# Kernel optimization log

Hardware: AMD Instinct MI355X
Metric: run time of the kernel (lower is better)

The kernel has to match this reference:

```python
import jax, jax.numpy as jnp
import numpy as np


def setup_inputs() -> dict:
    key = jax.random.key(0)
    ks = jax.random.split(key, 6)
    B, H, W, C = 4, 64, 64, 256
    D = 256  # d_model
    s = 0.02
    return {
        "features": jax.random.normal(ks[0], (B, H, W, C), dtype=jnp.float32),
        "Wq": jax.random.normal(ks[1], (C, D), dtype=jnp.float32) * s,
        "bq": jnp.zeros((D,), dtype=jnp.float32),
        "Wk": jax.random.normal(ks[2], (C, D), dtype=jnp.float32) * s,
        "bk": jnp.zeros((D,), dtype=jnp.float32),
        "Wv": jax.random.normal(ks[3], (C, D), dtype=jnp.float32) * s,
        "bv": jnp.zeros((D,), dtype=jnp.float32),
        "Wo": jax.random.normal(ks[4], (D, C), dtype=jnp.float32) * s,
        "bo": jnp.zeros((C,), dtype=jnp.float32),
    }


def reference(features, Wq, bq, Wk, bk, Wv, bv, Wo, bo):
    # features: [B, H, W, C] (NHWC). 1x1 convs are per-pixel GEMMs, so flatten
    # spatial dims to N = H*W tokens and do single-head self-attention.
    B, H, W, C = features.shape
    D = Wq.shape[1]
    x = features.reshape(B, H * W, C)          # [B, N, C]
    q = x @ Wq + bq                            # [B, N, D]
    k = x @ Wk + bk                            # [B, N, D]
    v = x @ Wv + bv                            # [B, N, D]
    scale = np.float32(1.0 / np.sqrt(D))
    scores = jnp.einsum("bnd,bmd->bnm", q, k) * scale   # [B, N, N]
    attn = jax.nn.softmax(scores, axis=-1)               # [B, N, N]
    out = jnp.einsum("bnm,bmd->bnd", attn, v)            # [B, N, D]
    out = out @ Wo + bo                                  # [B, N, C]
    return out.reshape(B, H, W, C)
```

## Files before the change

### kernel.cpp

```cpp
#include <hip/hip_runtime.h>
#include <hip/hip_bf16.h>


typedef __attribute__((ext_vector_type(8))) short short8;
typedef __attribute__((ext_vector_type(4))) short short4v;
typedef __attribute__((ext_vector_type(4))) float floatx4;

#define NB 4
#define NT 4096
#define CD 256
#define MTOT (NB * NT)

__device__ __forceinline__ short bf16s(float f) {
    union { float f; unsigned u; } a; a.f = f;
    unsigned u = a.u;
    return (short)((u + 0x7fffu + ((u >> 16) & 1u)) >> 16);
}

__device__ __forceinline__ float bf2f(short s) {
    union { unsigned u; float f; } a;
    a.u = ((unsigned)(unsigned short)s) << 16;
    return a.f;
}

__device__ __forceinline__ short8 ld8(const short* p) {
    return *(const short8*)p;
}

__device__ __forceinline__ floatx4 mfma16(short8 a, short8 b, floatx4 c) {
    return __builtin_amdgcn_mfma_f32_16x16x32_bf16(a, b, c, 0, 0, 0);
}

__device__ __forceinline__ void dma16(const void* g, void* l) {
    __builtin_amdgcn_global_load_lds(
        (const __attribute__((address_space(1))) void*)g,
        (__attribute__((address_space(3))) void*)l, 16, 0, 0);
}

__global__ __launch_bounds__(256) void k_convx(const float* __restrict__ x,
                                               short* __restrict__ xb) {
    int i = (blockIdx.x * 256 + threadIdx.x) * 4;
    float4 v = *(const float4*)(x + i);
    short4v o;
    o.x = bf16s(v.x); o.y = bf16s(v.y); o.z = bf16s(v.z); o.w = bf16s(v.w);
    *(short4v*)(xb + i) = o;
}

__global__ __launch_bounds__(256) void k_convw(const float* __restrict__ w0,
                                               const float* __restrict__ w1,
                                               const float* __restrict__ w2,
                                               const float* __restrict__ w3,
                                               short* __restrict__ wt) {
    int z = blockIdx.y;
    const float* w = (z == 0) ? w0 : (z == 1) ? w1 : (z == 2) ? w2 : w3;
    int c = blockIdx.x;
    int n = threadIdx.x;
    wt[z * 65536 + n * 256 + c] = bf16s(w[c * 256 + n]);
}

__global__ __launch_bounds__(256) void k_proj3(const short* __restrict__ A,
                                               const short* __restrict__ Wt,
                                               const float* __restrict__ bq,
                                               const float* __restrict__ bk,
                                               const float* __restrict__ bv,
                                               short* __restrict__ Qb,
                                               short* __restrict__ Kb,
                                               short* __restrict__ Vt) {
    __shared__ __align__(16) short Ws[16384];
    int blk = blockIdx.x;
    int wk = (blk & 7) * 192 + (blk >> 3);
    int m = wk / 12, rest = wk - m * 12;
    int z = rest >> 2, y = rest & 3;
    const short* W = Wt + z * 65536;
    const float* bias = (z == 0) ? bq : (z == 1) ? bk : bv;
    float scale = (z == 0) ? 0.0625f : 1.0f;
    int m0 = m * 128;
    int n0 = y * 64;
    int tid = threadIdx.x;
    int w = tid >> 6, l = tid & 63, r = l & 15, q = l >> 4;

#pragma unroll
    for (int cg = 0; cg < 8; ++cg)
        dma16(W + (size_t)(n0 + w * 16 + r) * CD + (cg * 4 + q) * 8,
              &Ws[w * 4096 + cg * 512]);
    __syncthreads();

    const short* a0 = A + (size_t)(m0 + w * 32 + r) * CD;
    const short* a1 = a0 + 16 * CD;
    floatx4 acc[2][4];
#pragma unroll
    for (int rt = 0; rt < 2; ++rt)
#pragma unroll
        for (int j = 0; j < 4; ++j) acc[rt][j] = (floatx4){0.f, 0.f, 0.f, 0.f};
#pragma unroll
    for (int c = 0; c < 8; ++c) {
        short8 af0 = ld8(a0 + c * 32 + q * 8);
        short8 af1 = ld8(a1 + c * 32 + q * 8);
#pragma unroll
        for (int j = 0; j < 4; ++j) {
            short8 wf = ld8(&Ws[j * 4096 + c * 512 + l * 8]);
            acc[0][j] = mfma16(af0, wf, acc[0][j]);
            acc[1][j] = mfma16(af1, wf, acc[1][j]);
        }
    }
#pragma unroll
    for (int rt = 0; rt < 2; ++rt)
#pragma unroll
        for (int j = 0; j < 4; ++j) {
            int col = n0 + j * 16 + r;
            float bvv = bias[col];
#pragma unroll
            for (int i = 0; i < 4; ++i) {
                int row = m0 + w * 32 + rt * 16 + q * 4 + i;
                short s = bf16s((acc[rt][j][i] + bvv) * scale);
                if (z == 0) Qb[(size_t)row * CD + col] = s;
                else if (z == 1) Kb[(size_t)row * CD + col] = s;
                else {
                    int bb = row >> 12, lm = row & (NT - 1);
                    Vt[((size_t)bb * CD + col) * NT + lm] = s;
                }
            }
        }
}

__global__ __launch_bounds__(256, 3) void k_attn(const short* __restrict__ Qb,
                                                 const short* __restrict__ Kb,
                                                 const short* __restrict__ Vt,
                                                 short* __restrict__ Op0,
                                                 short* __restrict__ Op1,
                                                 short* __restrict__ Op2,
                                                 float* __restrict__ Lp,
                                                 int nks) {
    __shared__ __align__(16) short Ks[2][8192];
    __shared__ __align__(16) short P[64][36];

    const int tid = threadIdx.x;
    const int w = tid >> 6;
    const int l = tid & 63;
    const int r = l & 15, q = l >> 4;
    const int nbk = gridDim.x;
    const int blk = blockIdx.x;
    const int wk = (blk & 7) * (nbk >> 3) + (blk >> 3);
    const int bx = wk & 63;
    const int co = wk >> 6;
    const int b = co / nks;
    const int ks = co - b * nks;
    const int m0 = bx * 64;
    const int qq = 128 / nks, rem = 128 % nks;
    const int u0 = ks * qq + (ks < rem ? ks : rem);
    const int cnt = qq + (ks < rem ? 1 : 0);
    const int t0 = u0 * 32;
    const int tt_d = w & 1;
    const int cb_d = (w >> 1) * 4;
    const short* Qp = Qb + (size_t)b * NT * CD;
    const short* Kp = Kb + (size_t)b * NT * CD;
    const short* Vp = Vt + (size_t)b * CD * NT;
    short* Op = (ks == 0) ? Op0 : (ks == 1) ? Op1 : Op2;

    short8 qf[8];
#pragma unroll
    for (int c = 0; c < 8; ++c)
        qf[c] = ld8(Qp + (size_t)(m0 + w * 16 + r) * CD + c * 32 + q * 8);

    floatx4 o[4][4];
#pragma unroll
    for (int rt = 0; rt < 4; ++rt)
#pragma unroll
        for (int dt = 0; dt < 4; ++dt) o[rt][dt] = (floatx4){0.f, 0.f, 0.f, 0.f};
    float ls = 0.f;

#pragma unroll
    for (int j = 0; j < 4; ++j)
        dma16(Kp + (size_t)(t0 + tt_d * 16 + r) * CD + ((cb_d + j) * 4 + q) * 8,
              &Ks[0][tt_d * 4096 + (cb_d + j) * 512]);

#pragma unroll 1
    for (int it = 0; it < cnt; ++it) {
        const int p = it & 1;
        const int n0 = t0 + it * 32;
        __syncthreads();

        short8 vf[4];
#pragma unroll
        for (int dt = 0; dt < 4; ++dt)
            vf[dt] = ld8(Vp + (size_t)(w * 64 + dt * 16 + r) * NT + n0 + q * 8);

        if (it + 1 < cnt) {
#pragma unroll
            for (int j = 0; j < 4; ++j)
                dma16(Kp + (size_t)(n0 + 32 + tt_d * 16 + r) * CD + ((cb_d + j) * 4 + q) * 8,
                      &Ks[1 - p][tt_d * 4096 + (cb_d + j) * 512]);
        }

        floatx4 s0 = {0.f, 0.f, 0.f, 0.f};
        floatx4 s1 = {0.f, 0.f, 0.f, 0.f};
#pragma unroll
        for (int c = 0; c < 8; ++c) {
            s0 = mfma16(ld8(&Ks[p][c * 512 + l * 8]), qf[c], s0);
            s1 = mfma16(ld8(&Ks[p][4096 + c * 512 + l * 8]), qf[c], s1);
        }

#pragma unroll
        for (int tt = 0; tt < 2; ++tt) {
            floatx4 sv = tt ? s1 : s0;
            float e0 = __expf(sv[0]), e1 = __expf(sv[1]);
            float e2 = __expf(sv[2]), e3 = __expf(sv[3]);
            ls += (e0 + e1) + (e2 + e3);
            unsigned pk01, pk23;
            asm("v_cvt_pk_bf16_f32 %0, %1, %2" : "=v"(pk01) : "v"(e0), "v"(e1));
            asm("v_cvt_pk_bf16_f32 %0, %1, %2" : "=v"(pk23) : "v"(e2), "v"(e3));
            uint2 pk; pk.x = pk01; pk.y = pk23;
            *(uint2*)&P[w * 16 + r][tt * 16 + q * 4] = pk;
        }
        asm volatile("s_waitcnt lgkmcnt(0)\n\ts_barrier" ::: "memory");

#pragma unroll
        for (int rt = 0; rt < 4; ++rt) {
            short8 pf = ld8(&P[rt * 16 + r][q * 8]);
#pragma unroll
            for (int dt = 0; dt < 4; ++dt)
                o[rt][dt] = mfma16(pf, vf[dt], o[rt][dt]);
        }
    }

    ls += __shfl_xor(ls, 16);
    ls += __shfl_xor(ls, 32);
    if (l < 16)
        Lp[(size_t)ks * MTOT + b * NT + m0 + w * 16 + l] = ls;

#pragma unroll
    for (int rt = 0; rt < 4; ++rt)
#pragma unroll
        for (int i = 0; i < 4; ++i) {
            int row = m0 + rt * 16 + q * 4 + i;
#pragma unroll
            for (int dt = 0; dt < 4; ++dt)
                Op[((size_t)b * NT + row) * CD + w * 64 + dt * 16 + r] =
                    bf16s(o[rt][dt][i]);
        }
}

__global__ __launch_bounds__(256) void k_oproj(const short* __restrict__ Op0,
                                               const short* __restrict__ Op1,
                                               const short* __restrict__ Op2,
                                               const float* __restrict__ Lp,
                                               const short* __restrict__ Wot,
                                               const float* __restrict__ bo,
                                               float* __restrict__ out, int nks) {
    __shared__ __align__(16) short Ws[16384];
    int blk = blockIdx.x;
    int wk = (blk & 7) * 64 + (blk >> 3);
    int m0 = (wk >> 2) * 128;
    int n0 = (wk & 3) * 64;
    int tid = threadIdx.x;
    int w = tid >> 6, l = tid & 63, r = l & 15, q = l >> 4;

#pragma unroll
    for (int cg = 0; cg < 8; ++cg)
        dma16(Wot + (size_t)(n0 + w * 16 + r) * CD + (cg * 4 + q) * 8,
              &Ws[w * 4096 + cg * 512]);
    __syncthreads();

    int row0 = m0 + w * 32 + r;
    float lt0 = Lp[row0] + Lp[MTOT + row0];
    float lt1 = Lp[row0 + 16] + Lp[MTOT + row0 + 16];
    if (nks == 3) { lt0 += Lp[2 * (size_t)MTOT + row0]; lt1 += Lp[2 * (size_t)MTOT + row0 + 16]; }
    float inv0 = 1.0f / lt0, inv1 = 1.0f / lt1;
    const short* p0 = Op0 + (size_t)row0 * CD;
    const short* p1 = Op1 + (size_t)row0 * CD;
    const short* p2 = Op2 + (size_t)row0 * CD;
    floatx4 acc[2][4];
#pragma unroll
    for (int rt = 0; rt < 2; ++rt)
#pragma unroll
        for (int j = 0; j < 4; ++j) acc[rt][j] = (floatx4){0.f, 0.f, 0.f, 0.f};
#pragma unroll
    for (int c = 0; c < 8; ++c) {
        int off0 = c * 32 + q * 8, off1 = 16 * CD + c * 32 + q * 8;
        short8 x0 = ld8(p0 + off0), y0 = ld8(p1 + off0);
        short8 x1 = ld8(p0 + off1), y1 = ld8(p1 + off1);
        short8 af0, af1;
        if (nks == 3) {
            short8 z0 = ld8(p2 + off0), z1 = ld8(p2 + off1);
#pragma unroll
            for (int jj = 0; jj < 8; ++jj) {
                af0[jj] = bf16s((bf2f(x0[jj]) + bf2f(y0[jj]) + bf2f(z0[jj])) * inv0);
                af1[jj] = bf16s((bf2f(x1[jj]) + bf2f(y1[jj]) + bf2f(z1[jj])) * inv1);
            }
        } else {
#pragma unroll
            for (int jj = 0; jj < 8; ++jj) {
                af0[jj] = bf16s((bf2f(x0[jj]) + bf2f(y0[jj])) * inv0);
                af1[jj] = bf16s((bf2f(x1[jj]) + bf2f(y1[jj])) * inv1);
            }
        }
#pragma unroll
        for (int j = 0; j < 4; ++j) {
            short8 wf = ld8(&Ws[j * 4096 + c * 512 + l * 8]);
            acc[0][j] = mfma16(af0, wf, acc[0][j]);
            acc[1][j] = mfma16(af1, wf, acc[1][j]);
        }
    }
#pragma unroll
    for (int rt = 0; rt < 2; ++rt)
#pragma unroll
        for (int j = 0; j < 4; ++j) {
            int col = n0 + j * 16 + r;
            float bvv = bo[col];
#pragma unroll
            for (int i = 0; i < 4; ++i)
                out[(size_t)(m0 + w * 32 + rt * 16 + q * 4 + i) * CD + col] =
                    acc[rt][j][i] + bvv;
        }
}

extern "C" void kernel_launch(void* const* d_in, const int* in_sizes, int n_in,
                              void* d_out, int out_size, void* d_ws, size_t ws_size,
                              hipStream_t stream) {
    const float* x  = (const float*)d_in[0];
    const float* Wq = (const float*)d_in[1];
    const float* bq = (const float*)d_in[2];
    const float* Wk = (const float*)d_in[3];
    const float* bk = (const float*)d_in[4];
    const float* Wv = (const float*)d_in[5];
    const float* bv = (const float*)d_in[6];
    const float* Wo = (const float*)d_in[7];
    const float* bo = (const float*)d_in[8];
    float* out = (float*)d_out;

    char* ws = (char*)d_ws;
    const size_t MB = 1024u * 1024u;
    short* xb  = (short*)(ws);
    short* Op0 = (short*)(ws);
    short* Qb  = (short*)(ws + 8 * MB);
    short* Kb  = (short*)(ws + 16 * MB);
    short* Vt  = (short*)(ws + 24 * MB);
    short* Op1 = (short*)(ws + 32 * MB);
    short* Wt  = (short*)(ws + 40 * MB);
    float* Lp  = (float*)(ws + 40 * MB + 512 * 1024);
    short* Op2 = (short*)(ws + 41 * MB);

    int nks = (ws_size >= 49 * MB + 512 * 1024) ? 3 : 2;
    if (nks == 2) Op2 = Op1;

    k_convx<<<dim3(MTOT * CD / (256 * 4)), 256, 0, stream>>>(x, xb);
    k_convw<<<dim3(256, 4), 256, 0, stream>>>(Wq, Wk, Wv, Wo, Wt);
    k_proj3<<<dim3(1536), 256, 0, stream>>>(xb, Wt, bq, bk, bv, Qb, Kb, Vt);
    k_attn<<<dim3(64 * NB * nks), 256, 0, stream>>>(Qb, Kb, Vt, Op0, Op1, Op2, Lp, nks);
    k_oproj<<<dim3(512), 256, 0, stream>>>(Op0, Op1, Op2, Lp, Wt + 196608, bo, out, nks);
}
```

Before: 271.6 us.

## Process 64-key tiles per iteration with single K buffer; simplify block indexing

The attention loop now handles 64 keys per iteration instead of 32, with a single 32KB K tile in shared memory in place of the double-buffered pair. The prefetch of the next K tile is issued after the score barrier so it overlaps the P·V MFMAs, halving the barrier count per key. V loads are split into two halves, and the projection kernels drop the XCD-swizzled block remapping in favour of plain 2D/3D grids. The trade-offs are a K-load latency exposed at the top of each iteration instead of fully hidden by double buffering, more registers for the extra V fragments, and possibly worse L2 locality across XCDs in the projections.

```diff
diff --git a/kernel.cpp b/kernel.cpp
--- a/kernel.cpp
+++ b/kernel.cpp
@@ -67,15 +67,12 @@
                                                short* __restrict__ Kb,
                                                short* __restrict__ Vt) {
     __shared__ __align__(16) short Ws[16384];
-    int blk = blockIdx.x;
-    int wk = (blk & 7) * 192 + (blk >> 3);
-    int m = wk / 12, rest = wk - m * 12;
-    int z = rest >> 2, y = rest & 3;
+    int z = blockIdx.z;
     const short* W = Wt + z * 65536;
     const float* bias = (z == 0) ? bq : (z == 1) ? bk : bv;
     float scale = (z == 0) ? 0.0625f : 1.0f;
-    int m0 = m * 128;
-    int n0 = y * 64;
+    int m0 = blockIdx.x * 128;
+    int n0 = blockIdx.y * 64;
     int tid = threadIdx.x;
     int w = tid >> 6, l = tid & 63, r = l & 15, q = l >> 4;
 
@@ -131,8 +128,8 @@
                                                  short* __restrict__ Op2,
                                                  float* __restrict__ Lp,
                                                  int nks) {
-    __shared__ __align__(16) short Ks[2][8192];
-    __shared__ __align__(16) short P[64][36];
+    __shared__ __align__(16) short Ks[16384];
+    __shared__ __align__(16) short P[64][68];
 
     const int tid = threadIdx.x;
     const int w = tid >> 6;
@@ -146,12 +143,10 @@
     const int b = co / nks;
     const int ks = co - b * nks;
     const int m0 = bx * 64;
-    const int qq = 128 / nks, rem = 128 % nks;
+    const int qq = 64 / nks, rem = 64 % nks;
     const int u0 = ks * qq + (ks < rem ? ks : rem);
     const int cnt = qq + (ks < rem ? 1 : 0);
-    const int t0 = u0 * 32;
-    const int tt_d = w & 1;
-    const int cb_d = (w >> 1) * 4;
+    const int t0 = u0 * 64;
     const short* Qp = Qb + (size_t)b * NT * CD;
     const short* Kp = Kb + (size_t)b * NT * CD;
     const short* Vp = Vt + (size_t)b * CD * NT;
@@ -170,56 +165,90 @@
     float ls = 0.f;
 
 #pragma unroll
-    for (int j = 0; j < 4; ++j)
-        dma16(Kp + (size_t)(t0 + tt_d * 16 + r) * CD + ((cb_d + j) * 4 + q) * 8,
-              &Ks[0][tt_d * 4096 + (cb_d + j) * 512]);
+    for (int j = 0; j < 8; ++j)
+        dma16(Kp + (size_t)(t0 + w * 16 + r) * CD + (j * 4 + q) * 8,
+              &Ks[w * 4096 + j * 512]);
 
 #pragma unroll 1
     for (int it = 0; it < cnt; ++it) {
-        const int p = it & 1;
-        const int n0 = t0 + it * 32;
+        const int n0 = t0 + it * 64;
         __syncthreads();
 
-        short8 vf[4];
+        short8 va[4];
 #pragma unroll
         for (int dt = 0; dt < 4; ++dt)
-            vf[dt] = ld8(Vp + (size_t)(w * 64 + dt * 16 + r) * NT + n0 + q * 8);
+            va[dt] = ld8(Vp + (size_t)(w * 64 + dt * 16 + r) * NT + n0 + q * 8);
+
+        {
+            floatx4 s0 = {0.f, 0.f, 0.f, 0.f};
+            floatx4 s1 = {0.f, 0.f, 0.f, 0.f};
+#pragma unroll
+            for (int c = 0; c < 8; ++c) {
+                s0 = mfma16(ld8(&Ks[c * 512 + l * 8]), qf[c], s0);
+                s1 = mfma16(ld8(&Ks[4096 + c * 512 + l * 8]), qf[c], s1);
+            }
+#pragma unroll
+            for (int tt = 0; tt < 2; ++tt) {
+                floatx4 sv = tt ? s1 : s0;
+                float e0 = __expf(sv[0]), e1 = __expf(sv[1]);
+                float e2 = __expf(sv[2]), e3 = __expf(sv[3]);
+                ls += (e0 + e1) + (e2 + e3);
+                unsigned pk01, pk23;
+                asm("v_cvt_pk_bf16_f32 %0, %1, %2" : "=v"(pk01) : "v"(e0), "v"(e1));
+                asm("v_cvt_pk_bf16_f32 %0, %1, %2" : "=v"(pk23) : "v"(e2), "v"(e3));
+                uint2 pk; pk.x = pk01; pk.y = pk23;
+                *(uint2*)&P[w * 16 + r][tt * 16 + q * 4] = pk;
+            }
+        }
+        {
+            floatx4 s2 = {0.f, 0.f, 0.f, 0.f};
+            floatx4 s3 = {0.f, 0.f, 0.f, 0.f};
+#pragma unroll
+            for (int c = 0; c < 8; ++c) {
+                s2 = mfma16(ld8(&Ks[8192 + c * 512 + l * 8]), qf[c], s2);
+                s3 = mfma16(ld8(&Ks[12288 + c * 512 + l * 8]), qf[c], s3);
+            }
+#pragma unroll
+            for (int tt = 0; tt < 2; ++tt) {
+                floatx4 sv = tt ? s3 : s2;
+                float e0 = __expf(sv[0]), e1 = __expf(sv[1]);
+                float e2 = __expf(sv[2]), e3 = __expf(sv[3]);
+                ls += (e0 + e1) + (e2 + e3);
+                unsigned pk01, pk23;
+                asm("v_cvt_pk_bf16_f32 %0, %1, %2" : "=v"(pk01) : "v"(e0), "v"(e1));
+                asm("v_cvt_pk_bf16_f32 %0, %1, %2" : "=v"(pk23) : "v"(e2), "v"(e3));
+                uint2 pk; pk.x = pk01; pk.y = pk23;
+                *(uint2*)&P[w * 16 + r][32 + tt * 16 + q * 4] = pk;
+            }
+        }
+
+        asm volatile("s_waitcnt lgkmcnt(0)\n\ts_barrier" ::: "memory");
 
         if (it + 1 < cnt) {
 #pragma unroll
-            for (int j = 0; j < 4; ++j)
-                dma16(Kp + (size_t)(n0 + 32 + tt_d * 16 + r) * CD + ((cb_d + j) * 4 + q) * 8,
-                      &Ks[1 - p][tt_d * 4096 + (cb_d + j) * 512]);
-        }
-
-        floatx4 s0 = {0.f, 0.f, 0.f, 0.f};
-        floatx4 s1 = {0.f, 0.f, 0.f, 0.f};
-#pragma unroll
-        for (int c = 0; c < 8; ++c) {
-            s0 = mfma16(ld8(&Ks[p][c * 512 + l * 8]), qf[c], s0);
-            s1 = mfma16(ld8(&Ks[p][4096 + c * 512 + l * 8]), qf[c], s1);
-        }
-
-#pragma unroll
-        for (int tt = 0; tt < 2; ++tt) {
-            floatx4 sv = tt ? s1 : s0;
-            float e0 = __expf(sv[0]), e1 = __expf(sv[1]);
-            float e2 = __expf(sv[2]), e3 = __expf(sv[3]);
-            ls += (e0 + e1) + (e2 + e3);
-            unsigned pk01, pk23;
-            asm("v_cvt_pk_bf16_f32 %0, %1, %2" : "=v"(pk01) : "v"(e0), "v"(e1));
-            asm("v_cvt_pk_bf16_f32 %0, %1, %2" : "=v"(pk23) : "v"(e2), "v"(e3));
-            uint2 pk; pk.x = pk01; pk.y = pk23;
-            *(uint2*)&P[w * 16 + r][tt * 16 + q * 4] = pk;
-        }
-        asm volatile("s_waitcnt lgkmcnt(0)\n\ts_barrier" ::: "memory");
+            for (int j = 0; j < 8; ++j)
+                dma16(Kp + (size_t)(n0 + 64 + w * 16 + r) * CD + (j * 4 + q) * 8,
+                      &Ks[w * 4096 + j * 512]);
+        }
+
+        short8 vb[4];
+#pragma unroll
+        for (int dt = 0; dt < 4; ++dt)
+            vb[dt] = ld8(Vp + (size_t)(w * 64 + dt * 16 + r) * NT + n0 + 32 + q * 8);
 
 #pragma unroll
         for (int rt = 0; rt < 4; ++rt) {
             short8 pf = ld8(&P[rt * 16 + r][q * 8]);
 #pragma unroll
             for (int dt = 0; dt < 4; ++dt)
-                o[rt][dt] = mfma16(pf, vf[dt], o[rt][dt]);
+                o[rt][dt] = mfma16(pf, va[dt], o[rt][dt]);
+        }
+#pragma unroll
+        for (int rt = 0; rt < 4; ++rt) {
+            short8 pf = ld8(&P[rt * 16 + r][32 + q * 8]);
+#pragma unroll
+            for (int dt = 0; dt < 4; ++dt)
+                o[rt][dt] = mfma16(pf, vb[dt], o[rt][dt]);
         }
     }
 
@@ -248,10 +277,8 @@
                                                const float* __restrict__ bo,
                                                float* __restrict__ out, int nks) {
     __shared__ __align__(16) short Ws[16384];
-    int blk = blockIdx.x;
-    int wk = (blk & 7) * 64 + (blk >> 3);
-    int m0 = (wk >> 2) * 128;
-    int n0 = (wk & 3) * 64;
+    int m0 = blockIdx.x * 128;
+    int n0 = blockIdx.y * 64;
     int tid = threadIdx.x;
     int w = tid >> 6, l = tid & 63, r = l & 15, q = l >> 4;
 
@@ -345,7 +372,7 @@
 
     k_convx<<<dim3(MTOT * CD / (256 * 4)), 256, 0, stream>>>(x, xb);
     k_convw<<<dim3(256, 4), 256, 0, stream>>>(Wq, Wk, Wv, Wo, Wt);
-    k_proj3<<<dim3(1536), 256, 0, stream>>>(xb, Wt, bq, bk, bv, Qb, Kb, Vt);
+    k_proj3<<<dim3(MTOT / 128, CD / 64, 3), 256, 0, stream>>>(xb, Wt, bq, bk, bv, Qb, Kb, Vt);
     k_attn<<<dim3(64 * NB * nks), 256, 0, stream>>>(Qb, Kb, Vt, Op0, Op1, Op2, Lp, nks);
-    k_oproj<<<dim3(512), 256, 0, stream>>>(Op0, Op1, Op2, Lp, Wt + 196608, bo, out, nks);
-}
+    k_oproj<<<dim3(MTOT / 128, CD / 64), 256, 0, stream>>>(Op0, Op1, Op2, Lp, Wt + 196608, bo, out, nks);
+}
```

Result: no change. 269.4 us (-0.8%).

## Keep P in registers via lane shuffles, drop LDS P tile and barrier

Applied to the files above, without the earlier changes.

The attention kernel no longer stages the exponentiated score tile P through shared memory behind a barrier. Each wave now rebuilds its own P fragment in registers with cross-lane shuffles and multiplies it against all 256 value columns, holding 16 accumulators per wave instead of splitting columns across waves. V loads are software-pipelined in groups of four. Each wave now streams the full V tile, so global V traffic per block rises and register pressure grows, and the XCD-aware block swizzles in the projection kernels are replaced by plain 2D/3D grids.

```diff
diff --git a/kernel.cpp b/kernel.cpp
--- a/kernel.cpp
+++ b/kernel.cpp
@@ -67,15 +67,12 @@
                                                short* __restrict__ Kb,
                                                short* __restrict__ Vt) {
     __shared__ __align__(16) short Ws[16384];
-    int blk = blockIdx.x;
-    int wk = (blk & 7) * 192 + (blk >> 3);
-    int m = wk / 12, rest = wk - m * 12;
-    int z = rest >> 2, y = rest & 3;
+    int z = blockIdx.z;
     const short* W = Wt + z * 65536;
     const float* bias = (z == 0) ? bq : (z == 1) ? bk : bv;
     float scale = (z == 0) ? 0.0625f : 1.0f;
-    int m0 = m * 128;
-    int n0 = y * 64;
+    int m0 = blockIdx.x * 128;
+    int n0 = blockIdx.y * 64;
     int tid = threadIdx.x;
     int w = tid >> 6, l = tid & 63, r = l & 15, q = l >> 4;
 
@@ -132,12 +129,12 @@
                                                  float* __restrict__ Lp,
                                                  int nks) {
     __shared__ __align__(16) short Ks[2][8192];
-    __shared__ __align__(16) short P[64][36];
 
     const int tid = threadIdx.x;
     const int w = tid >> 6;
     const int l = tid & 63;
     const int r = l & 15, q = l >> 4;
+    const int pb = ((q & 1) << 1) | (q >> 1);
     const int nbk = gridDim.x;
     const int blk = blockIdx.x;
     const int wk = (blk & 7) * (nbk >> 3) + (blk >> 3);
@@ -162,11 +159,9 @@
     for (int c = 0; c < 8; ++c)
         qf[c] = ld8(Qp + (size_t)(m0 + w * 16 + r) * CD + c * 32 + q * 8);
 
-    floatx4 o[4][4];
-#pragma unroll
-    for (int rt = 0; rt < 4; ++rt)
-#pragma unroll
-        for (int dt = 0; dt < 4; ++dt) o[rt][dt] = (floatx4){0.f, 0.f, 0.f, 0.f};
+    floatx4 o[16];
+#pragma unroll
+    for (int dt = 0; dt < 16; ++dt) o[dt] = (floatx4){0.f, 0.f, 0.f, 0.f};
     float ls = 0.f;
 
 #pragma unroll
@@ -180,11 +175,6 @@
         const int n0 = t0 + it * 32;
         __syncthreads();
 
-        short8 vf[4];
-#pragma unroll
-        for (int dt = 0; dt < 4; ++dt)
-            vf[dt] = ld8(Vp + (size_t)(w * 64 + dt * 16 + r) * NT + n0 + q * 8);
-
         if (it + 1 < cnt) {
 #pragma unroll
             for (int j = 0; j < 4; ++j)
@@ -192,6 +182,12 @@
                       &Ks[1 - p][tt_d * 4096 + (cb_d + j) * 512]);
         }
 
+        const short* vbase = Vp + n0 + pb * 8 + (size_t)r * NT;
+        short8 vfp[4], vfn[4];
+#pragma unroll
+        for (int u = 0; u < 4; ++u)
+            vfp[u] = ld8(vbase + (size_t)(u * 16) * NT);
+
         floatx4 s0 = {0.f, 0.f, 0.f, 0.f};
         floatx4 s1 = {0.f, 0.f, 0.f, 0.f};
 #pragma unroll
@@ -200,26 +196,40 @@
             s1 = mfma16(ld8(&Ks[p][4096 + c * 512 + l * 8]), qf[c], s1);
         }
 
-#pragma unroll
-        for (int tt = 0; tt < 2; ++tt) {
-            floatx4 sv = tt ? s1 : s0;
-            float e0 = __expf(sv[0]), e1 = __expf(sv[1]);
-            float e2 = __expf(sv[2]), e3 = __expf(sv[3]);
-            ls += (e0 + e1) + (e2 + e3);
-            unsigned pk01, pk23;
-            asm("v_cvt_pk_bf16_f32 %0, %1, %2" : "=v"(pk01) : "v"(e0), "v"(e1));
-            asm("v_cvt_pk_bf16_f32 %0, %1, %2" : "=v"(pk23) : "v"(e2), "v"(e3));
-            uint2 pk; pk.x = pk01; pk.y = pk23;
-            *(uint2*)&P[w * 16 + r][tt * 16 + q * 4] = pk;
-        }
-        asm volatile("s_waitcnt lgkmcnt(0)\n\ts_barrier" ::: "memory");
-
-#pragma unroll
-        for (int rt = 0; rt < 4; ++rt) {
-            short8 pf = ld8(&P[rt * 16 + r][q * 8]);
-#pragma unroll
-            for (int dt = 0; dt < 4; ++dt)
-                o[rt][dt] = mfma16(pf, vf[dt], o[rt][dt]);
+        float a0 = __expf(s0[0]), a1 = __expf(s0[1]);
+        float a2 = __expf(s0[2]), a3 = __expf(s0[3]);
+        float b0 = __expf(s1[0]), b1 = __expf(s1[1]);
+        float b2 = __expf(s1[2]), b3 = __expf(s1[3]);
+        ls += (a0 + a1) + (a2 + a3) + (b0 + b1) + (b2 + b3);
+        unsigned pk00, pk01, pk10, pk11;
+        asm("v_cvt_pk_bf16_f32 %0, %1, %2" : "=v"(pk00) : "v"(a0), "v"(a1));
+        asm("v_cvt_pk_bf16_f32 %0, %1, %2" : "=v"(pk01) : "v"(a2), "v"(a3));
+        asm("v_cvt_pk_bf16_f32 %0, %1, %2" : "=v"(pk10) : "v"(b0), "v"(b1));
+        asm("v_cvt_pk_bf16_f32 %0, %1, %2" : "=v"(pk11) : "v"(b2), "v"(b3));
+
+        unsigned sw0 = (q & 1) ? pk00 : pk10;
+        unsigned sw1 = (q & 1) ? pk01 : pk11;
+        unsigned rw0 = __shfl_xor(sw0, 16);
+        unsigned rw1 = __shfl_xor(sw1, 16);
+        union { unsigned u[4]; short8 v; } pu;
+        pu.u[0] = (q & 1) ? rw0 : pk00;
+        pu.u[1] = (q & 1) ? rw1 : pk01;
+        pu.u[2] = (q & 1) ? pk10 : rw0;
+        pu.u[3] = (q & 1) ? pk11 : rw1;
+        short8 pfv = pu.v;
+
+#pragma unroll
+        for (int g = 0; g < 4; ++g) {
+            if (g < 3) {
+#pragma unroll
+                for (int u = 0; u < 4; ++u)
+                    vfn[u] = ld8(vbase + (size_t)((g + 1) * 4 + u) * 16 * NT);
+            }
+#pragma unroll
+            for (int u = 0; u < 4; ++u)
+                o[g * 4 + u] = mfma16(pfv, vfp[u], o[g * 4 + u]);
+#pragma unroll
+            for (int u = 0; u < 4; ++u) vfp[u] = vfn[u];
         }
     }
 
@@ -229,14 +239,11 @@
         Lp[(size_t)ks * MTOT + b * NT + m0 + w * 16 + l] = ls;
 
 #pragma unroll
-    for (int rt = 0; rt < 4; ++rt)
+    for (int dt = 0; dt < 16; ++dt)
 #pragma unroll
         for (int i = 0; i < 4; ++i) {
-            int row = m0 + rt * 16 + q * 4 + i;
-#pragma unroll
-            for (int dt = 0; dt < 4; ++dt)
-                Op[((size_t)b * NT + row) * CD + w * 64 + dt * 16 + r] =
-                    bf16s(o[rt][dt][i]);
+            int row = m0 + w * 16 + q * 4 + i;
+            Op[((size_t)b * NT + row) * CD + dt * 16 + r] = bf16s(o[dt][i]);
         }
 }
 
@@ -248,10 +255,8 @@
                                                const float* __restrict__ bo,
                                                float* __restrict__ out, int nks) {
     __shared__ __align__(16) short Ws[16384];
-    int blk = blockIdx.x;
-    int wk = (blk & 7) * 64 + (blk >> 3);
-    int m0 = (wk >> 2) * 128;
-    int n0 = (wk & 3) * 64;
+    int m0 = blockIdx.x * 128;
+    int n0 = blockIdx.y * 64;
     int tid = threadIdx.x;
     int w = tid >> 6, l = tid & 63, r = l & 15, q = l >> 4;
 
@@ -345,7 +350,7 @@
 
     k_convx<<<dim3(MTOT * CD / (256 * 4)), 256, 0, stream>>>(x, xb);
     k_convw<<<dim3(256, 4), 256, 0, stream>>>(Wq, Wk, Wv, Wo, Wt);
-    k_proj3<<<dim3(1536), 256, 0, stream>>>(xb, Wt, bq, bk, bv, Qb, Kb, Vt);
+    k_proj3<<<dim3(MTOT / 128, CD / 64, 3), 256, 0, stream>>>(xb, Wt, bq, bk, bv, Qb, Kb, Vt);
     k_attn<<<dim3(64 * NB * nks), 256, 0, stream>>>(Qb, Kb, Vt, Op0, Op1, Op2, Lp, nks);
-    k_oproj<<<dim3(512), 256, 0, stream>>>(Op0, Op1, Op2, Lp, Wt + 196608, bo, out, nks);
-}
+    k_oproj<<<dim3(MTOT / 128, CD / 64), 256, 0, stream>>>(Op0, Op1, Op2, Lp, Wt + 196608, bo, out, nks);
+}
```

New measurement: 417.2 us. 1.54x slower.
